# Kernel optimization log

Measured on AMD Instinct MI355X. Metric: run time of the kernel, lower is better.

Reference implementation:

```python
import jax, jax.numpy as jnp
import numpy as np
import math

DIM = 2048
H = 16
KV = 4
HD = DIM // H  # 128
ROPE_DIM = 64  # head_dim * rope_fraction(0.5), even
ROPE_BASE = 10000.0
EPS_RMS = 1.1920928955078125e-07  # torch fp32 finfo eps (F.rms_norm default)


def rms_norm(t):
    # F.rms_norm over last dim, no weight
    return t * jax.lax.rsqrt(jnp.mean(t * t, axis=-1, keepdims=True) + EPS_RMS)


def rope_tables(seqlen, dtype):
    inv_freq = 1.0 / (ROPE_BASE ** (jnp.arange(0, ROPE_DIM, 2, dtype=jnp.float32) / ROPE_DIM))
    t = jnp.arange(seqlen, dtype=jnp.float32)
    freqs = jnp.outer(t, inv_freq)  # [S, ROPE_DIM//2]
    return jnp.cos(freqs).astype(dtype)[None, None], jnp.sin(freqs).astype(dtype)[None, None]


def apply_partial_rope(x, cos, sin):
    # x: [B, h, S, HD]; rotate first ROPE_DIM dims, pass through the rest
    xr = x[..., :ROPE_DIM]
    half = ROPE_DIM // 2
    x1, x2 = xr[..., :half], xr[..., half:]
    rotated = jnp.concatenate((x1 * cos + x2 * sin, -x1 * sin + x2 * cos), axis=-1)
    return jnp.concatenate((rotated, x[..., ROPE_DIM:]), axis=-1)


def setup_inputs() -> dict:
    key = jax.random.key(0)
    ks = jax.random.split(key, 5)
    B, S = 4, 1024
    x = jax.random.normal(ks[0], (B, S, DIM), dtype=jnp.float32)
    Wq = jax.random.normal(ks[1], (DIM, DIM), dtype=jnp.float32) * 0.02
    Wk = jax.random.normal(ks[2], (KV * HD, DIM), dtype=jnp.float32) * 0.02
    Wv = jax.random.normal(ks[3], (KV * HD, DIM), dtype=jnp.float32) * 0.02
    Wproj = jax.random.normal(ks[4], (DIM, DIM), dtype=jnp.float32) * 0.02
    # causal boolean mask [B, S, S]
    causal = jnp.tril(jnp.ones((S, S), dtype=bool))
    attn_mask = jnp.broadcast_to(causal[None], (B, S, S))
    return {"x": x, "attn_mask": attn_mask, "Wq": Wq, "Wk": Wk, "Wv": Wv, "Wproj": Wproj}


def reference(x, attn_mask, Wq, Wk, Wv, Wproj):
    B, S, D = x.shape
    repeat = H // KV
    q = (x @ Wq.T).reshape(B, S, H, HD).transpose(0, 2, 1, 3)   # [B,H,S,HD]
    k = (x @ Wk.T).reshape(B, S, KV, HD).transpose(0, 2, 1, 3)  # [B,KV,S,HD]
    v = (x @ Wv.T).reshape(B, S, KV, HD).transpose(0, 2, 1, 3)
    q = rms_norm(q)
    k = rms_norm(k)
    cos, sin = rope_tables(S, q.dtype)
    q = apply_partial_rope(q, cos, sin)
    k = apply_partial_rope(k, cos, sin)
    # GQA: expand kv heads
    k_rep = jnp.repeat(k, repeat, axis=1)  # [B,H,S,HD]
    v_rep = jnp.repeat(v, repeat, axis=1)
    bias = jnp.where(attn_mask[:, None], jnp.float32(0.0), jnp.float32(-10000.0)).astype(q.dtype)
    scores = jnp.einsum('bhqd,bhkd->bhqk', q, k_rep) / math.sqrt(HD) + bias
    attn = jax.nn.softmax(scores, axis=-1)
    y = jnp.einsum('bhqk,bhkd->bhqd', attn, v_rep)
    valid = jnp.any(attn_mask, axis=-1)[:, None, :, None].astype(y.dtype)
    y = y * valid
    # xsa: remove component of y along self value vector
    denom = jnp.maximum(jnp.sum(v_rep * v_rep, axis=-1, keepdims=True), 1e-06)
    proj = jnp.sum(y * v_rep, axis=-1, keepdims=True) / denom
    y = y - proj * v_rep
    y = y.transpose(0, 2, 1, 3).reshape(B, S, D)
    return y @ Wproj.T
```

## Files before the change

### kernel.cpp

```cpp
#include <hip/hip_runtime.h>


typedef __attribute__((ext_vector_type(8))) __bf16 bf16x8;
typedef __attribute__((ext_vector_type(4))) __bf16 bf16x4;
typedef __attribute__((ext_vector_type(4))) float f32x4;

static_assert(sizeof(__bf16) == 2, "bf16 size");

#define MFMA16x16x32(a, b, c) __builtin_amdgcn_mfma_f32_16x16x32_bf16((a), (b), (c), 0, 0, 0)

#if __has_builtin(__builtin_amdgcn_exp2f)
#define EXP2(x) __builtin_amdgcn_exp2f(x)
#else
#define EXP2(x) exp2f(x)
#endif

__device__ __forceinline__ void gload_lds16(const void* g, void* l) {
  __builtin_amdgcn_global_load_lds((const __attribute__((address_space(1))) void*)g,
                                   (__attribute__((address_space(3))) void*)l, 16, 0, 0);
}

__global__ __launch_bounds__(256) void prep(const float* __restrict__ x,
                                            const float* __restrict__ wq,
                                            const float* __restrict__ wk,
                                            const float* __restrict__ wv,
                                            const float* __restrict__ wp,
                                            __bf16* __restrict__ xb,
                                            __bf16* __restrict__ wb,
                                            __bf16* __restrict__ wpb,
                                            float2* __restrict__ tab) {
  constexpr int NX = 2097152;
  constexpr int NW1 = 1048576;
  constexpr int NW2 = 262144;
  constexpr int NP = 1048576;
  constexpr int NT = 32768;
  constexpr int TOT = NX + NW1 + 2 * NW2 + NP + NT;
  auto cast4 = [](const float* s, __bf16* d, int i) {
    f32x4 v = ((const f32x4*)s)[i];
    bf16x4 o;
    o[0] = (__bf16)v[0];
    o[1] = (__bf16)v[1];
    o[2] = (__bf16)v[2];
    o[3] = (__bf16)v[3];
    ((bf16x4*)d)[i] = o;
  };
  int i = blockIdx.x * blockDim.x + threadIdx.x;
  const int stride = gridDim.x * blockDim.x;
  for (; i < TOT; i += stride) {
    int j = i;
    if (j < NX) {
      cast4(x, xb, j);
    } else if ((j -= NX) < NW1) {
      cast4(wq, wb, j);
    } else if ((j -= NW1) < NW2) {
      cast4(wk, wb + (size_t)NW1 * 4, j);
    } else if ((j -= NW2) < NW2) {
      cast4(wv, wb + (size_t)(NW1 + NW2) * 4, j);
    } else if ((j -= NW2) < NP) {
      cast4(wp, wpb, j);
    } else {
      j -= NP;
      const int s = j >> 5, jj = j & 31;
      const float inv = powf(10000.0f, -(float)jj * 0.03125f);
      const float ang = (float)s * inv;
      tab[j] = make_float2(cosf(ang), sinf(ang));
    }
  }
}

template <typename CT, bool FUSE>
__global__ __launch_bounds__(256) void gemm_bt(const __bf16* __restrict__ A,
                                               const __bf16* __restrict__ B,
                                               CT* __restrict__ C, int N, int K, int nbn,
                                               const float2* __restrict__ tab) {
  __shared__ __bf16 As[2][128 * 32];
  __shared__ __bf16 Bs[2][128 * 32];
  const int nwg = gridDim.x;
  const int id = blockIdx.x;
  const int xid = (id & 7) * (nwg >> 3) + (id >> 3);
  const int bm = xid / nbn;
  const int bn = xid - bm * nbn;
  const int t = threadIdx.x;
  const int l = t & 63, w = t >> 6;
  const int wr = w >> 1, wc = w & 1;
  const int lr = l & 15, lk = l >> 4;
  const __bf16* Ab = A + (size_t)bm * 128 * K;
  const __bf16* Bb = B + (size_t)bn * 128 * K;
  const int srow = t >> 2;
  const int scol = ((t & 3) ^ ((srow >> 1) & 3)) << 3;
  f32x4 acc[4][4] = {};

  auto stage = [&](int k0, int buf) {
    gload_lds16(Ab + (size_t)srow * K + k0 + scol, &As[buf][t * 8]);
    gload_lds16(Ab + (size_t)(srow + 64) * K + k0 + scol, &As[buf][2048 + t * 8]);
    gload_lds16(Bb + (size_t)srow * K + k0 + scol, &Bs[buf][t * 8]);
    gload_lds16(Bb + (size_t)(srow + 64) * K + k0 + scol, &Bs[buf][2048 + t * 8]);
  };

  stage(0, 0);
  __syncthreads();

  const int NT = K >> 5;
  for (int kt = 0; kt < NT; ++kt) {
    const int cur = kt & 1;
    if (kt + 1 < NT) stage((kt + 1) << 5, cur ^ 1);

    bf16x8 af[4], bfr[4];
#pragma unroll
    for (int m = 0; m < 4; ++m) {
      const int row = wr * 64 + m * 16 + lr;
      af[m] = *(const bf16x8*)&As[cur][row * 32 + ((lk ^ ((row >> 1) & 3)) << 3)];
    }
#pragma unroll
    for (int n = 0; n < 4; ++n) {
      const int row = wc * 64 + n * 16 + lr;
      bfr[n] = *(const bf16x8*)&Bs[cur][row * 32 + ((lk ^ ((row >> 1) & 3)) << 3)];
    }
#pragma unroll
    for (int m = 0; m < 4; ++m)
#pragma unroll
      for (int n = 0; n < 4; ++n) acc[m][n] = MFMA16x16x32(af[m], bfr[n], acc[m][n]);

    __syncthreads();
  }

  if constexpr (FUSE) {
    if (bn < 20) {
      __shared__ float Ls[2][128];
      float ssp[4][4];
#pragma unroll
      for (int m = 0; m < 4; ++m)
#pragma unroll
        for (int i = 0; i < 4; ++i) {
          float s = 0.0f;
#pragma unroll
          for (int n = 0; n < 4; ++n) s += acc[m][n][i] * acc[m][n][i];
#pragma unroll
          for (int off = 1; off < 16; off <<= 1) s += __shfl_xor(s, off);
          ssp[m][i] = s;
        }
      if (lr == 0) {
#pragma unroll
        for (int m = 0; m < 4; ++m)
#pragma unroll
          for (int i = 0; i < 4; ++i)
            Ls[wc][wr * 64 + m * 16 + lk * 4 + i] = ssp[m][i];
      }
      __syncthreads();
      const bool isq = (bn < 16);
      const float qs = isq ? 0.1275174457f : 1.0f;
#pragma unroll
      for (int m = 0; m < 4; ++m) {
#pragma unroll
        for (int i = 0; i < 4; ++i) {
          const int rl = wr * 64 + m * 16 + lk * 4 + i;
          const int rg = bm * 128 + rl;
          const float sc =
              rsqrtf((Ls[0][rl] + Ls[1][rl]) * (1.0f / 128.0f) +
                     1.1920928955078125e-07f) *
              qs;
          CT* Cr = C + (size_t)rg * N + bn * 128;
          if (wc == 0) {
            const int s = rg & 1023;
#pragma unroll
            for (int n = 0; n < 2; ++n) {
              const int j = n * 16 + lr;
              const float2 cs = tab[s * 32 + j];
              const float x1 = acc[m][n][i], x2 = acc[m][n + 2][i];
              Cr[j] = (CT)((x1 * cs.x + x2 * cs.y) * sc);
              Cr[j + 32] = (CT)((-x1 * cs.y + x2 * cs.x) * sc);
            }
          } else {
#pragma unroll
            for (int n = 0; n < 4; ++n)
              Cr[64 + n * 16 + lr] = (CT)(acc[m][n][i] * sc);
          }
        }
      }
      return;
    }
  }

#pragma unroll
  for (int m = 0; m < 4; ++m) {
    const int row0 = bm * 128 + wr * 64 + m * 16 + lk * 4;
#pragma unroll
    for (int n = 0; n < 4; ++n) {
      const int col = bn * 128 + wc * 64 + n * 16 + lr;
#pragma unroll
      for (int i = 0; i < 4; ++i) C[(size_t)(row0 + i) * N + col] = (CT)acc[m][n][i];
    }
  }
}

__global__ __launch_bounds__(256) void vtrans(const __bf16* __restrict__ qkv,
                                              __bf16* __restrict__ vt) {
  __shared__ __bf16 L[64 * 128];
  const int tile = blockIdx.x;
  const int st = tile & 15, bk = tile >> 4;
  const int b = bk >> 2, kvh = bk & 3;
  const int t = threadIdx.x;
  const int s0 = st * 64;
  const __bf16* src = qkv + ((size_t)(b * 1024 + s0)) * 3072 + 2560 + kvh * 128;
#pragma unroll
  for (int r = 0; r < 4; ++r) {
    const int off = r * 2048 + t * 8;
    const int s = off >> 7, d = off & 127;
    bf16x8 v = *(const bf16x8*)(src + (size_t)s * 3072 + d);
    *(bf16x8*)&L[s * 128 + (d ^ ((s & 7) << 3) ^ (((s >> 3) & 7) << 3))] = v;
  }
  __syncthreads();
  __bf16* dst = vt + (size_t)bk * 128 * 1024;
#pragma unroll
  for (int r = 0; r < 4; ++r) {
    const int off = r * 2048 + t * 8;
    const int d = off >> 6, sc = off & 63;
    bf16x8 v;
#pragma unroll
    for (int j = 0; j < 8; ++j) {
      const int s = sc + j;
      v[j] = L[s * 128 + (d ^ ((s & 7) << 3) ^ (((s >> 3) & 7) << 3))];
    }
    *(bf16x8*)&dst[(size_t)d * 1024 + ((s0 + sc) ^ ((d & 7) << 3))] = v;
  }
}

__global__ __launch_bounds__(512) void attn_fwd(const __bf16* __restrict__ qkv,
                                                const __bf16* __restrict__ vt,
                                                __bf16* __restrict__ y) {
  const int id = blockIdx.x;
  const int g = (id & 7) | (((id >> 3) & 1) << 3);
  const int b = g >> 2, kvh = g & 3;
  const int hi = (id >> 4) & 3;
  const int pr = (id >> 6) & 3;
  const int h = kvh * 4 + hi;

  const int t = threadIdx.x;
  const int l = t & 63, w = t >> 6;
  const int lr = l & 15, lk = l >> 4;
  const int lr8 = lr & 7;

  __shared__ __bf16 Ks[2][64 * 128];
  __shared__ __bf16 Vs[2][128 * 64];
  __shared__ __bf16 Ps[8][16 * 64];

  const size_t rb = (size_t)b * 1024;
  const __bf16* Kg0 = qkv + rb * 3072 + 2048 + kvh * 128;
  const __bf16* Vtb = vt + (size_t)(b * 4 + kvh) * 128 * 1024;

  const int koff0 = t * 8;
  const int krow0 = koff0 >> 7;
  const int kcol0 = (koff0 & 127) ^ ((krow0 & 7) << 3);
  const int koff1 = 4096 + t * 8;
  const int krow1 = koff1 >> 7;
  const int kcol1 = (koff1 & 127) ^ ((krow1 & 7) << 3);
  const int voff0 = t * 8, voff1 = 4096 + t * 8;

#pragma unroll 1
  for (int pass = 0; pass < 2; ++pass) {
    const int qt = pass ? (7 - pr) : pr;
    const int q0 = qt << 7;

    bf16x8 aq[4];
    {
      const __bf16* qrow = qkv + (rb + q0 + w * 16 + lr) * 3072 + h * 128 + lk * 8;
#pragma unroll
      for (int kk = 0; kk < 4; ++kk) aq[kk] = *(const bf16x8*)(qrow + kk * 32);
    }

    float m_i[4], l_i[4];
    f32x4 o[8] = {};
#pragma unroll
    for (int i = 0; i < 4; ++i) {
      m_i[i] = -1e30f;
      l_i[i] = 0.0f;
    }

    const int rowg0 = q0 + w * 16 + lk * 4;
    const int wmin = q0 + w * 16;
    const int wmax = wmin + 15;
    const int nt = 2 * qt + 2;

    gload_lds16(Kg0 + (size_t)krow0 * 3072 + kcol0, &Ks[0][0] + koff0);
    gload_lds16(Kg0 + (size_t)krow1 * 3072 + kcol1, &Ks[0][0] + koff1);
    gload_lds16(Vtb + (size_t)(voff0 >> 6) * 1024 + (voff0 & 63), &Vs[0][0] + voff0);
    gload_lds16(Vtb + (size_t)(voff1 >> 6) * 1024 + (voff1 & 63), &Vs[0][0] + voff1);
    __syncthreads();

    for (int tt = 0; tt < nt; ++tt) {
      const int kv0 = tt * 64;
      const int cur = tt & 1;
      if (tt + 1 < nt) {
        const int nkv = kv0 + 64;
        const __bf16* Kg = Kg0 + (size_t)nkv * 3072;
        __bf16* kd = &Ks[cur ^ 1][0];
        __bf16* vd = &Vs[cur ^ 1][0];
        gload_lds16(Kg + (size_t)krow0 * 3072 + kcol0, kd + koff0);
        gload_lds16(Kg + (size_t)krow1 * 3072 + kcol1, kd + koff1);
        gload_lds16(Vtb + (size_t)(voff0 >> 6) * 1024 + nkv + (voff0 & 63), vd + voff0);
        gload_lds16(Vtb + (size_t)(voff1 >> 6) * 1024 + nkv + (voff1 & 63), vd + voff1);
      }

      if (kv0 <= wmax) {
        f32x4 sacc[4] = {};
        __builtin_amdgcn_s_setprio(1);
#pragma unroll
        for (int kk = 0; kk < 4; ++kk) {
#pragma unroll
          for (int n = 0; n < 4; ++n) {
            const bf16x8 bk = *(const bf16x8*)&Ks[cur][(n * 16 + lr) * 128 +
                                                      ((kk * 32 + lk * 8) ^ (lr8 << 3))];
            sacc[n] = MFMA16x16x32(aq[kk], bk, sacc[n]);
          }
        }
        __builtin_amdgcn_s_setprio(0);

        float pm[4];
#pragma unroll
        for (int i = 0; i < 4; ++i) pm[i] = -1e30f;
        if (kv0 + 63 > wmin) {
#pragma unroll
          for (int n = 0; n < 4; ++n) {
            const int colg = kv0 + n * 16 + lr;
#pragma unroll
            for (int i = 0; i < 4; ++i) {
              if (colg > rowg0 + i) sacc[n][i] = -1e30f;
              pm[i] = fmaxf(pm[i], sacc[n][i]);
            }
          }
        } else {
#pragma unroll
          for (int n = 0; n < 4; ++n)
#pragma unroll
            for (int i = 0; i < 4; ++i) pm[i] = fmaxf(pm[i], sacc[n][i]);
        }
#pragma unroll
        for (int i = 0; i < 4; ++i) {
          pm[i] = fmaxf(pm[i], __shfl_xor(pm[i], 1));
          pm[i] = fmaxf(pm[i], __shfl_xor(pm[i], 2));
          pm[i] = fmaxf(pm[i], __shfl_xor(pm[i], 4));
          pm[i] = fmaxf(pm[i], __shfl_xor(pm[i], 8));
        }
        float alpha[4], rs[4];
#pragma unroll
        for (int i = 0; i < 4; ++i) {
          const float mn = fmaxf(m_i[i], pm[i]);
          alpha[i] = EXP2(m_i[i] - mn);
          m_i[i] = mn;
          rs[i] = 0.0f;
        }
#pragma unroll
        for (int n = 0; n < 4; ++n) {
#pragma unroll
          for (int i = 0; i < 4; ++i) {
            const float p = EXP2(sacc[n][i] - m_i[i]);
            rs[i] += p;
            const int prow = lk * 4 + i;
            Ps[w][prow * 64 + ((n * 16 + lr) ^ ((prow & 7) << 3))] = (__bf16)p;
          }
        }
#pragma unroll
        for (int i = 0; i < 4; ++i) {
          rs[i] += __shfl_xor(rs[i], 1);
          rs[i] += __shfl_xor(rs[i], 2);
          rs[i] += __shfl_xor(rs[i], 4);
          rs[i] += __shfl_xor(rs[i], 8);
          l_i[i] = l_i[i] * alpha[i] + rs[i];
        }
#pragma unroll
        for (int f = 0; f < 8; ++f)
#pragma unroll
          for (int i = 0; i < 4; ++i) o[f][i] *= alpha[i];

        __builtin_amdgcn_s_setprio(1);
#pragma unroll
        for (int ks = 0; ks < 2; ++ks) {
          const bf16x8 pa =
              *(const bf16x8*)&Ps[w][lr * 64 + ((ks * 32 + lk * 8) ^ (lr8 << 3))];
#pragma unroll
          for (int f = 0; f < 8; ++f) {
            const bf16x8 vb = *(const bf16x8*)&Vs[cur][(f * 16 + lr) * 64 +
                                                       ((ks * 32 + lk * 8) ^ (lr8 << 3))];
            o[f] = MFMA16x16x32(pa, vb, o[f]);
          }
        }
        __builtin_amdgcn_s_setprio(0);
      }

      __syncthreads();
    }

#pragma unroll
    for (int i = 0; i < 4; ++i) {
      const int sg = rowg0 + i;
      const size_t mg = rb + sg;
      const __bf16* vp = qkv + mg * 3072 + 2560 + kvh * 128;
      const float invl = 1.0f / l_i[i];
      float vvv[8], yvv[8];
      float dyv = 0.0f, dvv = 0.0f;
#pragma unroll
      for (int f = 0; f < 8; ++f) {
        const float vf = (float)vp[f * 16 + lr];
        const float yf = o[f][i] * invl;
        vvv[f] = vf;
        yvv[f] = yf;
        dyv += yf * vf;
        dvv += vf * vf;
      }
#pragma unroll
      for (int off = 1; off < 16; off <<= 1) {
        dyv += __shfl_xor(dyv, off);
        dvv += __shfl_xor(dvv, off);
      }
      const float proj = dyv / fmaxf(dvv, 1e-6f);
      __bf16* yp = y + mg * 2048 + h * 128;
#pragma unroll
      for (int f = 0; f < 8; ++f) yp[f * 16 + lr] = (__bf16)(yvv[f] - proj * vvv[f]);
    }
  }
}

extern "C" void kernel_launch(void* const* d_in, const int* in_sizes, int n_in,
                              void* d_out, int out_size, void* d_ws, size_t ws_size,
                              hipStream_t stream) {
  const float* x = (const float*)d_in[0];
  const float* Wq = (const float*)d_in[2];
  const float* Wk = (const float*)d_in[3];
  const float* Wv = (const float*)d_in[4];
  const float* Wp = (const float*)d_in[5];
  float* out = (float*)d_out;

  __bf16* xb = (__bf16*)d_ws;
  __bf16* Wb = xb + (size_t)4096 * 2048;
  __bf16* Wpb = Wb + (size_t)3072 * 2048;
  __bf16* qkv = Wpb + (size_t)2048 * 2048;
  __bf16* yb = qkv + (size_t)4096 * 3072;
  float2* tab = (float2*)(yb + (size_t)4096 * 2048);
  __bf16* vt = xb;

  prep<<<2048, 256, 0, stream>>>(x, Wq, Wk, Wv, Wp, xb, Wb, Wpb, tab);

  gemm_bt<__bf16, true><<<768, 256, 0, stream>>>(xb, Wb, qkv, 3072, 2048, 24, tab);
  vtrans<<<256, 256, 0, stream>>>(qkv, vt);
  attn_fwd<<<256, 512, 0, stream>>>(qkv, vt, yb);
  gemm_bt<float, false><<<512, 256, 0, stream>>>(yb, Wpb, out, 2048, 2048, 16, nullptr);
}
```

Before: 182.5 us.

## Replace QKV GEMM with 256x256 tile, 8-wave pipelined kernel with fused RMS/RoPE

Adds a dedicated QKV projection kernel that uses 256x256 output tiles with BK=64 and 8 waves of 512 threads. It stages A/B tiles in quarter pieces through direct global-to-LDS loads and interleaves LDS reads with MFMA phases, using explicit barriers, waitcnts and setprio. The fused RMS-norm and RoPE epilogue moves into this kernel and is removed from the generic GEMM template. The aim is higher arithmetic intensity and better overlap of loads with MFMA. The cost is a grid of only 192 blocks on 256 CUs, large LDS use, and fragile hand-tuned synchronization.

Result: slower. 196.6 us (+7.7%).

```diff
diff --git a/kernel.cpp b/kernel.cpp
--- a/kernel.cpp
+++ b/kernel.cpp
@@ -68,11 +68,220 @@
   }
 }
 
-template <typename CT, bool FUSE>
+__global__ __launch_bounds__(512) void gemm8p_qkv(const __bf16* __restrict__ A,
+                                                  const __bf16* __restrict__ B,
+                                                  __bf16* __restrict__ C, int N, int K,
+                                                  int nbn, const float2* __restrict__ tab) {
+  __shared__ __bf16 As[2][256 * 64];
+  __shared__ __bf16 Bs[2][256 * 64];
+
+  const int nwg = gridDim.x;
+  const int id = blockIdx.x;
+  const int xid = (id & 7) * (nwg >> 3) + (id >> 3);
+  const int bm = xid / nbn;
+  const int bn = xid - bm * nbn;
+
+  const int t = threadIdx.x;
+  const int l = t & 63, w = t >> 6;
+  const int wr = w >> 2, wc = w & 3;
+  const int lr = l & 15, lk = l >> 4;
+  const int swz = lr & 7;
+  const __bf16* Ab = A + (size_t)bm * 256 * K;
+  const __bf16* Bb = B + (size_t)bn * 256 * K;
+  const int NT = K >> 6;
+
+  auto stageHalf = [&](int kt, int h) {
+    const int buf = kt & 1;
+    const __bf16* src = (h < 2) ? Ab : Bb;
+    __bf16* dst = ((h < 2) ? &As[buf][0] : &Bs[buf][0]) + (h & 1) * 8192;
+    const int k0 = kt << 6;
+    const int rb0 = (h & 1) * 128;
+#pragma unroll
+    for (int r = 0; r < 2; ++r) {
+      const int row = rb0 + r * 64 + (t >> 3);
+      const int cs = ((t & 7) ^ (row & 7)) << 3;
+      gload_lds16(src + (size_t)row * K + k0 + cs, dst + r * 4096 + t * 8);
+    }
+  };
+
+  f32x4 acc[8][4] = {};
+  bf16x8 aR[4][2], bR[4][2];
+
+  stageHalf(0, 0);
+  stageHalf(0, 1);
+  stageHalf(0, 2);
+  stageHalf(0, 3);
+  stageHalf(1, 0);
+  stageHalf(1, 1);
+  stageHalf(1, 2);
+  asm volatile("s_waitcnt vmcnt(6)" ::: "memory");
+  __builtin_amdgcn_sched_barrier(0);
+  __builtin_amdgcn_s_barrier();
+
+  for (int kt = 0; kt < NT; ++kt) {
+    const int buf = kt & 1;
+
+#pragma unroll
+    for (int m = 0; m < 4; ++m)
+#pragma unroll
+      for (int kk = 0; kk < 2; ++kk) {
+        const int row = wr * 128 + m * 16 + lr;
+        aR[m][kk] = *(const bf16x8*)&As[buf][row * 64 + (((kk * 4 + lk) ^ swz) << 3)];
+      }
+#pragma unroll
+    for (int n = 0; n < 2; ++n)
+#pragma unroll
+      for (int kk = 0; kk < 2; ++kk) {
+        const int row = wc * 64 + n * 16 + lr;
+        bR[n][kk] = *(const bf16x8*)&Bs[buf][row * 64 + (((kk * 4 + lk) ^ swz) << 3)];
+      }
+    if (kt + 1 < NT) stageHalf(kt + 1, 3);
+    __builtin_amdgcn_s_barrier();
+    asm volatile("s_waitcnt lgkmcnt(0)" ::: "memory");
+    __builtin_amdgcn_sched_barrier(0);
+    __builtin_amdgcn_s_setprio(1);
+#pragma unroll
+    for (int m = 0; m < 4; ++m)
+#pragma unroll
+      for (int n = 0; n < 2; ++n)
+#pragma unroll
+        for (int kk = 0; kk < 2; ++kk)
+          acc[m][n] = MFMA16x16x32(aR[m][kk], bR[n][kk], acc[m][n]);
+    __builtin_amdgcn_s_setprio(0);
+    __builtin_amdgcn_s_barrier();
+
+#pragma unroll
+    for (int n = 0; n < 2; ++n)
+#pragma unroll
+      for (int kk = 0; kk < 2; ++kk) {
+        const int row = wc * 64 + (n + 2) * 16 + lr;
+        bR[n + 2][kk] = *(const bf16x8*)&Bs[buf][row * 64 + (((kk * 4 + lk) ^ swz) << 3)];
+      }
+    __builtin_amdgcn_s_barrier();
+    asm volatile("s_waitcnt lgkmcnt(0)" ::: "memory");
+    __builtin_amdgcn_sched_barrier(0);
+    __builtin_amdgcn_s_setprio(1);
+#pragma unroll
+    for (int m = 0; m < 4; ++m)
+#pragma unroll
+      for (int n = 0; n < 2; ++n)
+#pragma unroll
+        for (int kk = 0; kk < 2; ++kk)
+          acc[m][n + 2] = MFMA16x16x32(aR[m][kk], bR[n + 2][kk], acc[m][n + 2]);
+    __builtin_amdgcn_s_setprio(0);
+    __builtin_amdgcn_s_barrier();
+
+#pragma unroll
+    for (int m = 0; m < 4; ++m)
+#pragma unroll
+      for (int kk = 0; kk < 2; ++kk) {
+        const int row = wr * 128 + (m + 4) * 16 + lr;
+        aR[m][kk] = *(const bf16x8*)&As[buf][row * 64 + (((kk * 4 + lk) ^ swz) << 3)];
+      }
+    __builtin_amdgcn_s_barrier();
+    asm volatile("s_waitcnt lgkmcnt(0)" ::: "memory");
+    __builtin_amdgcn_sched_barrier(0);
+    __builtin_amdgcn_s_setprio(1);
+#pragma unroll
+    for (int m = 0; m < 4; ++m)
+#pragma unroll
+      for (int n = 0; n < 2; ++n)
+#pragma unroll
+        for (int kk = 0; kk < 2; ++kk)
+          acc[m + 4][n] = MFMA16x16x32(aR[m][kk], bR[n][kk], acc[m + 4][n]);
+    __builtin_amdgcn_s_setprio(0);
+    __builtin_amdgcn_s_barrier();
+
+    if (kt + 2 < NT) {
+      stageHalf(kt + 2, 0);
+      stageHalf(kt + 2, 1);
+      stageHalf(kt + 2, 2);
+    }
+    if (kt < NT - 2)
+      asm volatile("s_waitcnt vmcnt(6)" ::: "memory");
+    else
+      asm volatile("s_waitcnt vmcnt(0)" ::: "memory");
+    __builtin_amdgcn_sched_barrier(0);
+    __builtin_amdgcn_s_barrier();
+    __builtin_amdgcn_s_setprio(1);
+#pragma unroll
+    for (int m = 0; m < 4; ++m)
+#pragma unroll
+      for (int n = 0; n < 2; ++n)
+#pragma unroll
+        for (int kk = 0; kk < 2; ++kk)
+          acc[m + 4][n + 2] = MFMA16x16x32(aR[m][kk], bR[n + 2][kk], acc[m + 4][n + 2]);
+    __builtin_amdgcn_s_setprio(0);
+    __builtin_amdgcn_s_barrier();
+  }
+
+  __syncthreads();
+
+  if (bn < 10) {
+    float* Ls = (float*)&As[0][0];
+#pragma unroll
+    for (int m = 0; m < 8; ++m) {
+#pragma unroll
+      for (int i = 0; i < 4; ++i) {
+        float s = 0.0f;
+#pragma unroll
+        for (int n = 0; n < 4; ++n) s += acc[m][n][i] * acc[m][n][i];
+#pragma unroll
+        for (int off = 1; off < 16; off <<= 1) s += __shfl_xor(s, off);
+        if (lr == 0) Ls[wc * 256 + wr * 128 + m * 16 + lk * 4 + i] = s;
+      }
+    }
+    __syncthreads();
+    const bool isq = (bn < 8);
+    const float qs = isq ? 0.1275174457f : 1.0f;
+    const int hh = wc >> 1;
+#pragma unroll
+    for (int m = 0; m < 8; ++m) {
+#pragma unroll
+      for (int i = 0; i < 4; ++i) {
+        const int rl = wr * 128 + m * 16 + lk * 4 + i;
+        const int rg = bm * 256 + rl;
+        const float sc = rsqrtf((Ls[2 * hh * 256 + rl] + Ls[(2 * hh + 1) * 256 + rl]) *
+                                    (1.0f / 128.0f) +
+                                1.1920928955078125e-07f) *
+                         qs;
+        __bf16* Cr = C + (size_t)rg * N + bn * 256 + hh * 128;
+        if ((wc & 1) == 0) {
+          const int s = rg & 1023;
+#pragma unroll
+          for (int n = 0; n < 2; ++n) {
+            const int j = n * 16 + lr;
+            const float2 cs2 = tab[s * 32 + j];
+            const float x1 = acc[m][n][i], x2 = acc[m][n + 2][i];
+            Cr[j] = (__bf16)((x1 * cs2.x + x2 * cs2.y) * sc);
+            Cr[j + 32] = (__bf16)((-x1 * cs2.y + x2 * cs2.x) * sc);
+          }
+        } else {
+#pragma unroll
+          for (int n = 0; n < 4; ++n)
+            Cr[64 + n * 16 + lr] = (__bf16)(acc[m][n][i] * sc);
+        }
+      }
+    }
+  } else {
+#pragma unroll
+    for (int m = 0; m < 8; ++m) {
+      const int row0 = bm * 256 + wr * 128 + m * 16 + lk * 4;
+#pragma unroll
+      for (int n = 0; n < 4; ++n) {
+        const int col = bn * 256 + wc * 64 + n * 16 + lr;
+#pragma unroll
+        for (int i = 0; i < 4; ++i)
+          C[(size_t)(row0 + i) * N + col] = (__bf16)acc[m][n][i];
+      }
+    }
+  }
+}
+
+template <typename CT>
 __global__ __launch_bounds__(256) void gemm_bt(const __bf16* __restrict__ A,
                                                const __bf16* __restrict__ B,
-                                               CT* __restrict__ C, int N, int K, int nbn,
-                                               const float2* __restrict__ tab) {
+                                               CT* __restrict__ C, int N, int K, int nbn) {
   __shared__ __bf16 As[2][128 * 32];
   __shared__ __bf16 Bs[2][128 * 32];
   const int nwg = gridDim.x;
@@ -124,63 +333,6 @@
     __syncthreads();
   }
 
-  if constexpr (FUSE) {
-    if (bn < 20) {
-      __shared__ float Ls[2][128];
-      float ssp[4][4];
-#pragma unroll
-      for (int m = 0; m < 4; ++m)
-#pragma unroll
-        for (int i = 0; i < 4; ++i) {
-          float s = 0.0f;
-#pragma unroll
-          for (int n = 0; n < 4; ++n) s += acc[m][n][i] * acc[m][n][i];
-#pragma unroll
-          for (int off = 1; off < 16; off <<= 1) s += __shfl_xor(s, off);
-          ssp[m][i] = s;
-        }
-      if (lr == 0) {
-#pragma unroll
-        for (int m = 0; m < 4; ++m)
-#pragma unroll
-          for (int i = 0; i < 4; ++i)
-            Ls[wc][wr * 64 + m * 16 + lk * 4 + i] = ssp[m][i];
-      }
-      __syncthreads();
-      const bool isq = (bn < 16);
-      const float qs = isq ? 0.1275174457f : 1.0f;
-#pragma unroll
-      for (int m = 0; m < 4; ++m) {
-#pragma unroll
-        for (int i = 0; i < 4; ++i) {
-          const int rl = wr * 64 + m * 16 + lk * 4 + i;
-          const int rg = bm * 128 + rl;
-          const float sc =
-              rsqrtf((Ls[0][rl] + Ls[1][rl]) * (1.0f / 128.0f) +
-                     1.1920928955078125e-07f) *
-              qs;
-          CT* Cr = C + (size_t)rg * N + bn * 128;
-          if (wc == 0) {
-            const int s = rg & 1023;
-#pragma unroll
-            for (int n = 0; n < 2; ++n) {
-              const int j = n * 16 + lr;
-              const float2 cs = tab[s * 32 + j];
-              const float x1 = acc[m][n][i], x2 = acc[m][n + 2][i];
-              Cr[j] = (CT)((x1 * cs.x + x2 * cs.y) * sc);
-              Cr[j + 32] = (CT)((-x1 * cs.y + x2 * cs.x) * sc);
-            }
-          } else {
-#pragma unroll
-            for (int n = 0; n < 4; ++n)
-              Cr[64 + n * 16 + lr] = (CT)(acc[m][n][i] * sc);
-          }
-        }
-      }
-      return;
-    }
-  }
-
 #pragma unroll
   for (int m = 0; m < 4; ++m) {
     const int row0 = bm * 128 + wr * 64 + m * 16 + lk * 4;
@@ -440,8 +592,8 @@
 
   prep<<<2048, 256, 0, stream>>>(x, Wq, Wk, Wv, Wp, xb, Wb, Wpb, tab);
 
-  gemm_bt<__bf16, true><<<768, 256, 0, stream>>>(xb, Wb, qkv, 3072, 2048, 24, tab);
+  gemm8p_qkv<<<192, 512, 0, stream>>>(xb, Wb, qkv, 3072, 2048, 12, tab);
   vtrans<<<256, 256, 0, stream>>>(qkv, vt);
   attn_fwd<<<256, 512, 0, stream>>>(qkv, vt, yb);
-  gemm_bt<float, false><<<512, 256, 0, stream>>>(yb, Wpb, out, 2048, 2048, 16, nullptr);
-}
+  gemm_bt<float><<<512, 256, 0, stream>>>(yb, Wpb, out, 2048, 2048, 16);
+}
```
